# Kernel optimization log

Measured on AMD Instinct MI355X. Metric: run time of the kernel, lower is better.

## Reference

```python
import jax, jax.numpy as jnp
import numpy as np

N = 4096      # atoms
K = 5         # atoms gathered per cell (top_k in put_atoms_in_cells)
M = 8         # neighbors kept per atom
NBR = 26      # neighbor cells per cell (9+9+8)

def _grid():
    # get_cells: box [-10,10) step 1 Angstrom -> 20^3 = 8000 cells
    g = jnp.arange(-10.0, 10.0, 1.0)
    X = jnp.stack(jnp.meshgrid(g, g, g))       # (3,20,20,20), tf.meshgrid default 'xy'
    return jnp.transpose(X).reshape(-1, 3)      # (8000,3)

def _sqdist(a, b):
    # ||a_i - b_j||^2 via expansion; avoids (A,B,3) intermediate
    return (jnp.sum(a * a, 1)[:, None] + jnp.sum(b * b, 1)[None, :] - 2.0 * (a @ b.T))

def _neighbor_list(coords):
    cells = _grid()                              # (n_cells, 3)
    # put_atoms_in_cells: tf.nn.top_k(norm, k) -> k LARGEST norms (faithful to source)
    d_ca = _sqdist(cells, coords)                # (n_cells, N)
    _, atoms_in_cells = jax.lax.top_k(d_ca, K)   # (n_cells, K)
    # get_cells_for_atoms: top_k(-norm, 1) -> closest cell per atom
    d_ac = _sqdist(coords, cells)                # (N, n_cells)
    cells_for_atoms = jnp.argmin(d_ac, axis=1)   # (N,)
    # compute_neighbor_cells: top_k(norm, 26) (faithful to source)
    d_cc = _sqdist(cells, cells)                 # (n_cells, n_cells)
    _, nbr_cells = jax.lax.top_k(d_cc, NBR)      # (n_cells, 26)
    nbr_cells_atom = nbr_cells[cells_for_atoms]  # (N, 26)
    nbr_inds = atoms_in_cells[nbr_cells_atom]    # (N, 26, K)
    nbr_coords = coords[nbr_inds]                # (N, 26, K, 3)
    dists = jnp.sum((coords[:, None, None, :] - nbr_coords) ** 2, axis=-1)
    dists = dists.reshape(N, NBR * K)            # (N, 130)
    _, locs = jax.lax.top_k(dists, M)            # top_k(dists, M) as in source
    flat = nbr_inds.reshape(N, NBR * K)
    return jnp.take_along_axis(flat, locs, axis=1)   # (N, M) atom indices

def _energy(coords, vdw, weights, nrot, nbr):
    # d_ij = r_ij - R_i - R_j
    diff = coords[:, None, :] - coords[nbr]      # (N, M, 3)
    r = jnp.sqrt(jnp.sum(diff * diff, axis=-1) + 1e-12)
    d = r - vdw[:, None] - vdw[nbr]
    g1 = jnp.exp(-(d / 0.5) ** 2)
    g2 = jnp.exp(-((d - 3.0) / 2.0) ** 2)
    rep = jnp.where(d < 0.0, d * d, 0.0)
    hyd = jnp.where(d < 0.5, 1.0, jnp.where(d < 1.5, 1.5 - d, 0.0))
    hb = jnp.where(d < -0.7, 1.0, jnp.where(d < 0.0, -d / 0.7, 0.0))
    hval = (weights[0] * g1 + weights[1] * g2 + weights[2] * rep
            + weights[3] * hyd + weights[4] * hb)
    f = jnp.where(d < 8.0, hval, 0.0)            # cutoff at 8 Angstrom
    c = jnp.sum(f)
    return c / (1.0 + weights[5] * nrot[0])      # g(c, Nrot)

def setup_inputs() -> dict:
    key = jax.random.key(0)
    k1, k2, k3 = jax.random.split(key, 3)
    coords = jax.random.uniform(k1, (N, 3), jnp.float32, -10.0, 10.0)
    vdw = jax.random.uniform(k2, (N,), jnp.float32, 1.0, 2.0)
    weights = 0.3 * jax.random.normal(k3, (6,), jnp.float32)
    nrot = 8.0 * jnp.ones((1,), jnp.float32)
    return {"coords": coords, "vdw": vdw, "weights": weights, "nrot": nrot}

def reference(coords, vdw, weights, nrot):
    nbr = _neighbor_list(coords)
    return _energy(coords, vdw, weights, nrot, nbr)
```

## Files before the change

### kernel.cpp

```cpp
#include <hip/hip_runtime.h>
#include <stdint.h>

#define NATOMS 4096
#define NCELLS 8000
#define KTOP 5
#define MNBR 8
#define NBRC 26
#define HBINS 217
#define LSTMAX 512

__device__ __forceinline__ unsigned long long umax64(unsigned long long a, unsigned long long b) {
    return a > b ? a : b;
}
__device__ __forceinline__ unsigned long long umin64(unsigned long long a, unsigned long long b) {
    return a < b ? a : b;
}

__device__ __forceinline__ void cell_coords_i(int m, int& x, int& y, int& z) {
    int a = m / 400;
    int r = m - a * 400;
    int b = r / 20;
    int c = r - b * 20;
    x = b - 10; y = c - 10; z = a - 10;
}

__global__ __launch_bounds__(256) void k1_cells_nbr(const float* __restrict__ coords,
                                                    int* __restrict__ cellsForAtoms,
                                                    int* __restrict__ nbrTable,
                                                    int* __restrict__ neededFlag) {
    const int atom = blockIdx.x;
    const int t = threadIdx.x;
    const int lane = t & 63;

    __shared__ int sCi;
    __shared__ uint32_t h[HBINS];
    __shared__ int lst[LSTMAX];
    __shared__ int sV, cnt;

    if (t < HBINS) h[t] = 0;
    if (t == 0) cnt = 0;

    if (t < 64) {
        float ax = coords[atom * 3], ay = coords[atom * 3 + 1], az = coords[atom * 3 + 2];
        float sa = __fadd_rn(__fadd_rn(__fmul_rn(ax, ax), __fmul_rn(ay, ay)), __fmul_rn(az, az));

        int fx = (int)floorf(ax), fy = (int)floorf(ay), fz = (int)floorf(az);
        int vx = min(9, max(-10, fx - 1 + (lane & 3)));
        int vy = min(9, max(-10, fy - 1 + ((lane >> 2) & 3)));
        int vz = min(9, max(-10, fz - 1 + (lane >> 4)));
        int m = (vz + 10) * 400 + (vx + 10) * 20 + (vy + 10);

        float cx = (float)vx, cy = (float)vy, cz = (float)vz;
        float scell = (float)(vx * vx + vy * vy + vz * vz);
        float dot = __fadd_rn(__fadd_rn(__fmul_rn(ax, cx), __fmul_rn(ay, cy)), __fmul_rn(az, cz));
        float val = __fsub_rn(__fadd_rn(sa, scell), __fmul_rn(2.0f, dot));
        unsigned long long key = ((unsigned long long)__float_as_uint(val) << 32) | (unsigned int)m;

        for (int off = 32; off > 0; off >>= 1)
            key = umin64(key, (unsigned long long)__shfl_xor((long long)key, off));
        if (lane == 0) {
            int c = (int)(key & 0xFFFFFFFFull);
            cellsForAtoms[atom] = c;
            sCi = c;
        }
    }
    __syncthreads();

    const int ci = sCi;
    int xi, yi, zi;
    cell_coords_i(ci, xi, yi, zi);
    const int Lx = max(xi + 10, 9 - xi);
    const int Ly = max(yi + 10, 9 - yi);
    const int Lz = max(zi + 10, 9 - zi);

    int lo;
    {
        int px[3] = { Lx * Lx, (Lx - 1) * (Lx - 1), (Lx - 2) * (Lx - 2) };
        int py[3] = { Ly * Ly, (Ly - 1) * (Ly - 1), (Ly - 2) * (Ly - 2) };
        int pz[3] = { Lz * Lz, (Lz - 1) * (Lz - 1), (Lz - 2) * (Lz - 2) };
        int m1 = 0x7FFFFFFF, m2 = 0x7FFFFFFF;
#pragma unroll
        for (int a = 0; a < 3; ++a)
#pragma unroll
            for (int b = 0; b < 3; ++b)
#pragma unroll
                for (int c = 0; c < 3; ++c) {
                    int s = px[a] + py[b] + pz[c];
                    if (s < m1) { m2 = m1; m1 = s; }
                    else if (s < m2) m2 = s;
                }
        lo = m2;
    }

#pragma unroll
    for (int col = 0; col < 2; ++col) {
        int p = t + 256 * col;
        if (p < 400) {
            int bb = p / 20, cc = p - bb * 20;
            int dxv = xi - (bb - 10), dyv = yi - (cc - 10);
            int Dbc = dxv * dxv + dyv * dyv;
            int R = lo - Dbc;
            int aLoEnd = 19, aHiStart = 20;
            if (R > 0) {
                int t0 = (int)ceilf(sqrtf((float)R));
                if ((t0 - 1) * (t0 - 1) >= R) --t0;
                if (t0 * t0 < R) ++t0;
                aLoEnd = min(19, zi + 10 - t0);
                aHiStart = max(0, zi + 10 + t0);
            }
            for (int a = 0; a <= aLoEnd; ++a) {
                int dzv = zi - (a - 10);
                atomicAdd(&h[Dbc + dzv * dzv - lo], 1u);
            }
            for (int a = aHiStart; a < 20; ++a) {
                int dzv = zi - (a - 10);
                atomicAdd(&h[Dbc + dzv * dzv - lo], 1u);
            }
        }
    }
    __syncthreads();

    if (t < 64) {
        int c4[4];
        int cnt4 = 0;
#pragma unroll
        for (int k = 0; k < 4; ++k) {
            int b = (HBINS - 1) - (t * 4 + k);
            c4[k] = (b >= 0) ? (int)h[b] : 0;
            cnt4 += c4[k];
        }
        int incl = cnt4;
        for (int off = 1; off < 64; off <<= 1) {
            int v = __shfl_up(incl, off);
            if (lane >= off) incl += v;
        }
        int P = incl - cnt4;
        if (P < NBRC && incl >= NBRC) {
            int run = P;
#pragma unroll
            for (int k = 0; k < 4; ++k) {
                run += c4[k];
                if (run >= NBRC) { sV = lo + (HBINS - 1) - (t * 4 + k); break; }
            }
        }
    }
    __syncthreads();
    const int V = sV;

#pragma unroll
    for (int col = 0; col < 2; ++col) {
        int p = t + 256 * col;
        if (p < 400) {
            int bb = p / 20, cc = p - bb * 20;
            int dxv = xi - (bb - 10), dyv = yi - (cc - 10);
            int Dbc = dxv * dxv + dyv * dyv;
            int R = V - Dbc;
            int aLoEnd = 19, aHiStart = 20;
            if (R > 0) {
                int t0 = (int)ceilf(sqrtf((float)R));
                if ((t0 - 1) * (t0 - 1) >= R) --t0;
                if (t0 * t0 < R) ++t0;
                aLoEnd = min(19, zi + 10 - t0);
                aHiStart = max(0, zi + 10 + t0);
            }
            for (int a = 0; a <= aLoEnd; ++a) {
                int dzv = zi - (a - 10);
                int d = Dbc + dzv * dzv;
                int j = a * 400 + p;
                int q = atomicAdd(&cnt, 1);
                if (q < LSTMAX) lst[q] = (d << 13) | (8191 - j);
            }
            for (int a = aHiStart; a < 20; ++a) {
                int dzv = zi - (a - 10);
                int d = Dbc + dzv * dzv;
                int j = a * 400 + p;
                int q = atomicAdd(&cnt, 1);
                if (q < LSTMAX) lst[q] = (d << 13) | (8191 - j);
            }
        }
    }
    __syncthreads();

    int n = min(cnt, LSTMAX);
    if (t < 64) {
        for (int base = 0; base < n; base += 64) {
            int idx = base + t;
            int key = (idx < n) ? lst[idx] : -1;
            int rank = 0;
            for (int m = 0; m < n; ++m) rank += (lst[m] > key) ? 1 : 0;
            if (idx < n && rank < NBRC) {
                int j = 8191 - (key & 8191);
                nbrTable[ci * NBRC + rank] = j;
                neededFlag[j] = 1;
            }
        }
    }
}

__global__ __launch_bounds__(256) void k2_atoms(const float* __restrict__ coords,
                                                const int* __restrict__ neededFlag,
                                                int* __restrict__ atomsInCells) {
    const int i = blockIdx.x;
    if (neededFlag[i] != 1) return;
    __shared__ unsigned long long redB[4];
    const int t = threadIdx.x;
    const int lane = t & 63, wv = t >> 6;

    int xi_, yi_, zi_;
    cell_coords_i(i, xi_, yi_, zi_);
    const float cx = (float)xi_, cy = (float)yi_, cz = (float)zi_;
    const float scell = (float)(xi_ * xi_ + yi_ * yi_ + zi_ * zi_);

    unsigned long long keys[16];
#pragma unroll
    for (int s = 0; s < 16; ++s) {
        int j = t + 256 * s;
        float ax = coords[j * 3], ay = coords[j * 3 + 1], az = coords[j * 3 + 2];
        float sa = __fadd_rn(__fadd_rn(__fmul_rn(ax, ax), __fmul_rn(ay, ay)), __fmul_rn(az, az));
        float dot = __fadd_rn(__fadd_rn(__fmul_rn(cx, ax), __fmul_rn(cy, ay)), __fmul_rn(cz, az));
        float val = __fsub_rn(__fadd_rn(scell, sa), __fmul_rn(2.0f, dot));
        keys[s] = ((unsigned long long)__float_as_uint(val) << 32) | (unsigned int)(4095 - j);
    }

    for (int r = 0; r < KTOP; ++r) {
        unsigned long long best = 0ull;
#pragma unroll
        for (int s = 0; s < 16; ++s) best = umax64(best, keys[s]);
        for (int off = 32; off > 0; off >>= 1)
            best = umax64(best, (unsigned long long)__shfl_xor((long long)best, off));
        if (lane == 0) redB[wv] = best;
        __syncthreads();
        unsigned long long wbest = umax64(umax64(redB[0], redB[1]), umax64(redB[2], redB[3]));
        if (t == 0) atomsInCells[i * KTOP + r] = 4095 - (int)(wbest & 0xFFFFFFFFull);
#pragma unroll
        for (int s = 0; s < 16; ++s) if (keys[s] == wbest) keys[s] = 0ull;
        __syncthreads();
    }
}

__global__ __launch_bounds__(256) void k3_energy(const float* __restrict__ coords,
                                                 const float* __restrict__ vdw,
                                                 const float* __restrict__ weights,
                                                 const int* __restrict__ nbrTable,
                                                 const int* __restrict__ atomsInCells,
                                                 const int* __restrict__ cellsForAtoms,
                                                 float* __restrict__ partials) {
    const int wid = threadIdx.x >> 6;
    const int lane = threadIdx.x & 63;
    const int i = blockIdx.x * 4 + wid;

    const float xi = coords[i * 3], yi = coords[i * 3 + 1], zi = coords[i * 3 + 2];
    const int ci = cellsForAtoms[i];

    int cand[3];
    unsigned long long keys[3];
#pragma unroll
    for (int s = 0; s < 3; ++s) {
        int p = lane + 64 * s;
        cand[s] = -1;
        keys[s] = 0ull;
        if (p < NBRC * KTOP) {
            int cellSlot = p / KTOP;
            int atomSlot = p - cellSlot * KTOP;
            int nc = nbrTable[ci * NBRC + cellSlot];
            int j = atomsInCells[nc * KTOP + atomSlot];
            cand[s] = j;
            float dx = __fsub_rn(xi, coords[j * 3]);
            float dy = __fsub_rn(yi, coords[j * 3 + 1]);
            float dz = __fsub_rn(zi, coords[j * 3 + 2]);
            float dist = __fadd_rn(__fadd_rn(__fmul_rn(dx, dx), __fmul_rn(dy, dy)), __fmul_rn(dz, dz));
            keys[s] = ((unsigned long long)__float_as_uint(dist) << 8) | (unsigned int)(255 - p);
        }
    }

    const float w0 = weights[0], w1 = weights[1], w2 = weights[2];
    const float w3 = weights[3], w4 = weights[4];
    const float vi = vdw[i];

    float esum = 0.0f;
    for (int r = 0; r < MNBR; ++r) {
        unsigned long long best = umax64(umax64(keys[0], keys[1]), keys[2]);
        for (int off = 32; off > 0; off >>= 1)
            best = umax64(best, (unsigned long long)__shfl_xor((long long)best, off));

        int p = 255 - (int)(best & 0xFFull);
        int slot = p >> 6;
        int owner = p & 63;
        int jsel = (slot == 0) ? cand[0] : (slot == 1) ? cand[1] : cand[2];
        int j = __shfl(jsel, owner);
        float dist = __uint_as_float((unsigned int)(best >> 8));

#pragma unroll
        for (int s = 0; s < 3; ++s) if (keys[s] == best) keys[s] = 0ull;

        float rr = __fsqrt_rn(__fadd_rn(dist, 1e-12f));
        float d = __fsub_rn(__fsub_rn(rr, vi), vdw[j]);
        float t1 = __fdiv_rn(d, 0.5f);
        float g1 = expf(-__fmul_rn(t1, t1));
        float t2 = __fdiv_rn(__fsub_rn(d, 3.0f), 2.0f);
        float g2 = expf(-__fmul_rn(t2, t2));
        float rep = (d < 0.0f) ? __fmul_rn(d, d) : 0.0f;
        float hyd = (d < 0.5f) ? 1.0f : ((d < 1.5f) ? __fsub_rn(1.5f, d) : 0.0f);
        float hb = (d < -0.7f) ? 1.0f : ((d < 0.0f) ? __fdiv_rn(-d, 0.7f) : 0.0f);
        float hval = __fadd_rn(__fadd_rn(__fadd_rn(__fadd_rn(
                         __fmul_rn(w0, g1), __fmul_rn(w1, g2)),
                         __fmul_rn(w2, rep)), __fmul_rn(w3, hyd)), __fmul_rn(w4, hb));
        float f = (d < 8.0f) ? hval : 0.0f;
        esum = __fadd_rn(esum, f);
    }
    if (lane == 0) partials[i] = esum;
}

__global__ __launch_bounds__(256) void k4_reduce(const float* __restrict__ partials,
                                                 const float* __restrict__ weights,
                                                 const float* __restrict__ nrot,
                                                 float* __restrict__ out) {
    __shared__ float red[256];
    const int t = threadIdx.x;
    float s = 0.0f;
    for (int k = 0; k < NATOMS / 256; ++k) s = __fadd_rn(s, partials[t + 256 * k]);
    red[t] = s;
    __syncthreads();
    for (int off = 128; off > 0; off >>= 1) {
        if (t < off) red[t] = __fadd_rn(red[t], red[t + off]);
        __syncthreads();
    }
    if (t == 0) out[0] = __fdiv_rn(red[0], __fadd_rn(1.0f, __fmul_rn(weights[5], nrot[0])));
}

extern "C" void kernel_launch(void* const* d_in, const int* in_sizes, int n_in,
                              void* d_out, int out_size, void* d_ws, size_t ws_size,
                              hipStream_t stream) {
    const float* coords  = (const float*)d_in[0];
    const float* vdw     = (const float*)d_in[1];
    const float* weights = (const float*)d_in[2];
    const float* nrot    = (const float*)d_in[3];
    float* out = (float*)d_out;

    int* nbrTable      = (int*)d_ws;
    int* atomsInCells  = nbrTable + NCELLS * NBRC;
    int* cellsForAtoms = atomsInCells + NCELLS * KTOP;
    int* neededFlag    = cellsForAtoms + NATOMS;
    float* partials    = (float*)(neededFlag + NCELLS);

    k1_cells_nbr<<<NATOMS, 256, 0, stream>>>(coords, cellsForAtoms, nbrTable, neededFlag);
    k2_atoms<<<NCELLS, 256, 0, stream>>>(coords, neededFlag, atomsInCells);
    k3_energy<<<NATOMS / 4, 256, 0, stream>>>(coords, vdw, weights, nbrTable,
                                              atomsInCells, cellsForAtoms, partials);
    k4_reduce<<<1, 256, 0, stream>>>(partials, weights, nrot, out);
}
```

Measured before the change: 42.56 us.

## Fuse final reduction into energy kernel, batch list atomics, cut k2 barriers

The final reduction kernel is folded into the energy kernel through a two-level atomic last-block counter, which removes one launch. The k1 candidate-list fill now does a wavefront prefix sum with one shared atomic per wave, replacing an atomic per element. k2 now computes a per-wave top-5 without block barriers and then merges the 20 wave winners by rank. The changes add acquire/release atomics and counter resets done in k1, and they must keep the tie-breaking order exact.

```diff
diff --git a/kernel.cpp b/kernel.cpp
--- a/kernel.cpp
+++ b/kernel.cpp
@@ -8,6 +8,7 @@
 #define NBRC 26
 #define HBINS 217
 #define LSTMAX 512
+#define K3GRPS 32
 
 __device__ __forceinline__ unsigned long long umax64(unsigned long long a, unsigned long long b) {
     return a > b ? a : b;
@@ -24,13 +25,27 @@
     x = b - 10; y = c - 10; z = a - 10;
 }
 
+__device__ __forceinline__ void a_ranges(int R, int zi, int& aLoEnd, int& aHiStart) {
+    aLoEnd = 19; aHiStart = 20;
+    if (R > 0) {
+        int t0 = (int)ceilf(sqrtf((float)R));
+        if ((t0 - 1) * (t0 - 1) >= R) --t0;
+        if (t0 * t0 < R) ++t0;
+        aLoEnd = min(19, zi + 10 - t0);
+        aHiStart = max(0, zi + 10 + t0);
+    }
+}
+
 __global__ __launch_bounds__(256) void k1_cells_nbr(const float* __restrict__ coords,
                                                     int* __restrict__ cellsForAtoms,
                                                     int* __restrict__ nbrTable,
-                                                    int* __restrict__ neededFlag) {
+                                                    int* __restrict__ neededFlag,
+                                                    int* __restrict__ cnts) {
     const int atom = blockIdx.x;
     const int t = threadIdx.x;
     const int lane = t & 63;
+
+    if (blockIdx.x == 0 && t < K3GRPS + 1) cnts[t] = 0;
 
     __shared__ int sCi;
     __shared__ uint32_t h[HBINS];
@@ -99,15 +114,8 @@
             int bb = p / 20, cc = p - bb * 20;
             int dxv = xi - (bb - 10), dyv = yi - (cc - 10);
             int Dbc = dxv * dxv + dyv * dyv;
-            int R = lo - Dbc;
-            int aLoEnd = 19, aHiStart = 20;
-            if (R > 0) {
-                int t0 = (int)ceilf(sqrtf((float)R));
-                if ((t0 - 1) * (t0 - 1) >= R) --t0;
-                if (t0 * t0 < R) ++t0;
-                aLoEnd = min(19, zi + 10 - t0);
-                aHiStart = max(0, zi + 10 + t0);
-            }
+            int aLoEnd, aHiStart;
+            a_ranges(lo - Dbc, zi, aLoEnd, aHiStart);
             for (int a = 0; a <= aLoEnd; ++a) {
                 int dzv = zi - (a - 10);
                 atomicAdd(&h[Dbc + dzv * dzv - lo], 1u);
@@ -150,33 +158,41 @@
 #pragma unroll
     for (int col = 0; col < 2; ++col) {
         int p = t + 256 * col;
+        int Dbc = 0, aLoEnd = -1, aHiStart = 20, cthr = 0;
         if (p < 400) {
             int bb = p / 20, cc = p - bb * 20;
             int dxv = xi - (bb - 10), dyv = yi - (cc - 10);
-            int Dbc = dxv * dxv + dyv * dyv;
-            int R = V - Dbc;
-            int aLoEnd = 19, aHiStart = 20;
-            if (R > 0) {
-                int t0 = (int)ceilf(sqrtf((float)R));
-                if ((t0 - 1) * (t0 - 1) >= R) --t0;
-                if (t0 * t0 < R) ++t0;
-                aLoEnd = min(19, zi + 10 - t0);
-                aHiStart = max(0, zi + 10 + t0);
-            }
-            for (int a = 0; a <= aLoEnd; ++a) {
-                int dzv = zi - (a - 10);
-                int d = Dbc + dzv * dzv;
-                int j = a * 400 + p;
-                int q = atomicAdd(&cnt, 1);
-                if (q < LSTMAX) lst[q] = (d << 13) | (8191 - j);
-            }
-            for (int a = aHiStart; a < 20; ++a) {
-                int dzv = zi - (a - 10);
-                int d = Dbc + dzv * dzv;
-                int j = a * 400 + p;
-                int q = atomicAdd(&cnt, 1);
-                if (q < LSTMAX) lst[q] = (d << 13) | (8191 - j);
-            }
+            Dbc = dxv * dxv + dyv * dyv;
+            a_ranges(V - Dbc, zi, aLoEnd, aHiStart);
+            int nlo = max(0, aLoEnd + 1);
+            int nhi = max(0, 20 - aHiStart);
+            cthr = nlo + nhi;
+        }
+        int incl = cthr;
+        for (int off = 1; off < 64; off <<= 1) {
+            int v = __shfl_up(incl, off);
+            if (lane >= off) incl += v;
+        }
+        int total = __shfl(incl, 63);
+        int base = 0;
+        if (total > 0) {
+            if (lane == 63) base = atomicAdd(&cnt, total);
+            base = __shfl(base, 63);
+        }
+        int w = base + (incl - cthr);
+        for (int a = 0; a <= aLoEnd; ++a) {
+            int dzv = zi - (a - 10);
+            int d = Dbc + dzv * dzv;
+            int j = a * 400 + p;
+            if (w < LSTMAX) lst[w] = (d << 13) | (8191 - j);
+            ++w;
+        }
+        for (int a = aHiStart; a < 20; ++a) {
+            int dzv = zi - (a - 10);
+            int d = Dbc + dzv * dzv;
+            int j = a * 400 + p;
+            if (w < LSTMAX) lst[w] = (d << 13) | (8191 - j);
+            ++w;
         }
     }
     __syncthreads();
@@ -202,7 +218,7 @@
                                                 int* __restrict__ atomsInCells) {
     const int i = blockIdx.x;
     if (neededFlag[i] != 1) return;
-    __shared__ unsigned long long redB[4];
+    __shared__ unsigned long long wl[4 * KTOP];
     const int t = threadIdx.x;
     const int lane = t & 63, wv = t >> 6;
 
@@ -228,26 +244,37 @@
         for (int s = 0; s < 16; ++s) best = umax64(best, keys[s]);
         for (int off = 32; off > 0; off >>= 1)
             best = umax64(best, (unsigned long long)__shfl_xor((long long)best, off));
-        if (lane == 0) redB[wv] = best;
-        __syncthreads();
-        unsigned long long wbest = umax64(umax64(redB[0], redB[1]), umax64(redB[2], redB[3]));
-        if (t == 0) atomsInCells[i * KTOP + r] = 4095 - (int)(wbest & 0xFFFFFFFFull);
-#pragma unroll
-        for (int s = 0; s < 16; ++s) if (keys[s] == wbest) keys[s] = 0ull;
-        __syncthreads();
-    }
-}
-
-__global__ __launch_bounds__(256) void k3_energy(const float* __restrict__ coords,
-                                                 const float* __restrict__ vdw,
-                                                 const float* __restrict__ weights,
-                                                 const int* __restrict__ nbrTable,
-                                                 const int* __restrict__ atomsInCells,
-                                                 const int* __restrict__ cellsForAtoms,
-                                                 float* __restrict__ partials) {
-    const int wid = threadIdx.x >> 6;
-    const int lane = threadIdx.x & 63;
+        if (lane == 0) wl[wv * KTOP + r] = best;
+#pragma unroll
+        for (int s = 0; s < 16; ++s) if (keys[s] == best) keys[s] = 0ull;
+    }
+    __syncthreads();
+
+    if (t < 4 * KTOP) {
+        unsigned long long key = wl[t];
+        int rank = 0;
+        for (int m = 0; m < 4 * KTOP; ++m) rank += (wl[m] > key) ? 1 : 0;
+        if (rank < KTOP) atomsInCells[i * KTOP + rank] = 4095 - (int)(key & 0xFFFFFFFFull);
+    }
+}
+
+__global__ __launch_bounds__(256) void k3_energy_red(const float* __restrict__ coords,
+                                                     const float* __restrict__ vdw,
+                                                     const float* __restrict__ weights,
+                                                     const float* __restrict__ nrot,
+                                                     const int* __restrict__ nbrTable,
+                                                     const int* __restrict__ atomsInCells,
+                                                     const int* __restrict__ cellsForAtoms,
+                                                     float* __restrict__ partials,
+                                                     int* __restrict__ cnts,
+                                                     float* __restrict__ out) {
+    const int t = threadIdx.x;
+    const int wid = t >> 6;
+    const int lane = t & 63;
     const int i = blockIdx.x * 4 + wid;
+
+    __shared__ int sIsLast;
+    __shared__ float red[256];
 
     const float xi = coords[i * 3], yi = coords[i * 3 + 1], zi = coords[i * 3 + 2];
     const int ci = cellsForAtoms[i];
@@ -309,23 +336,33 @@
         esum = __fadd_rn(esum, f);
     }
     if (lane == 0) partials[i] = esum;
-}
-
-__global__ __launch_bounds__(256) void k4_reduce(const float* __restrict__ partials,
-                                                 const float* __restrict__ weights,
-                                                 const float* __restrict__ nrot,
-                                                 float* __restrict__ out) {
-    __shared__ float red[256];
-    const int t = threadIdx.x;
-    float s = 0.0f;
-    for (int k = 0; k < NATOMS / 256; ++k) s = __fadd_rn(s, partials[t + 256 * k]);
-    red[t] = s;
-    __syncthreads();
-    for (int off = 128; off > 0; off >>= 1) {
-        if (t < off) red[t] = __fadd_rn(red[t], red[t + off]);
+
+    __syncthreads();
+    if (t == 0) {
+        int g = blockIdx.x >> 5;
+        int r = __hip_atomic_fetch_add(&cnts[g], 1, __ATOMIC_ACQ_REL,
+                                       __HIP_MEMORY_SCOPE_AGENT);
+        int last = 0;
+        if (r == 31) {
+            int f = __hip_atomic_fetch_add(&cnts[K3GRPS], 1, __ATOMIC_ACQ_REL,
+                                           __HIP_MEMORY_SCOPE_AGENT);
+            last = (f == K3GRPS - 1);
+        }
+        sIsLast = last;
+    }
+    __syncthreads();
+
+    if (sIsLast) {
+        float s = 0.0f;
+        for (int k = 0; k < NATOMS / 256; ++k) s = __fadd_rn(s, partials[t + 256 * k]);
+        red[t] = s;
         __syncthreads();
-    }
-    if (t == 0) out[0] = __fdiv_rn(red[0], __fadd_rn(1.0f, __fmul_rn(weights[5], nrot[0])));
+        for (int off = 128; off > 0; off >>= 1) {
+            if (t < off) red[t] = __fadd_rn(red[t], red[t + off]);
+            __syncthreads();
+        }
+        if (t == 0) out[0] = __fdiv_rn(red[0], __fadd_rn(1.0f, __fmul_rn(weights[5], nrot[0])));
+    }
 }
 
 extern "C" void kernel_launch(void* const* d_in, const int* in_sizes, int n_in,
@@ -342,10 +379,12 @@
     int* cellsForAtoms = atomsInCells + NCELLS * KTOP;
     int* neededFlag    = cellsForAtoms + NATOMS;
     float* partials    = (float*)(neededFlag + NCELLS);
-
-    k1_cells_nbr<<<NATOMS, 256, 0, stream>>>(coords, cellsForAtoms, nbrTable, neededFlag);
+    int* cnts          = (int*)(partials + NATOMS);
+
+    k1_cells_nbr<<<NATOMS, 256, 0, stream>>>(coords, cellsForAtoms, nbrTable,
+                                             neededFlag, cnts);
     k2_atoms<<<NCELLS, 256, 0, stream>>>(coords, neededFlag, atomsInCells);
-    k3_energy<<<NATOMS / 4, 256, 0, stream>>>(coords, vdw, weights, nbrTable,
-                                              atomsInCells, cellsForAtoms, partials);
-    k4_reduce<<<1, 256, 0, stream>>>(partials, weights, nrot, out);
-}
+    k3_energy_red<<<NATOMS / 4, 256, 0, stream>>>(coords, vdw, weights, nrot, nbrTable,
+                                                  atomsInCells, cellsForAtoms, partials,
+                                                  cnts, out);
+}
```

Result: slower. 59.06 us (+38.8%).
